# Performance work log

Measured on AMD Instinct MI355X. Metric: run time of the kernel, lower is better.

## Reference

```python
import jax, jax.numpy as jnp
import numpy as np

N_NODES = 100000
N_EDGES = 1600000
F_NODE = 32
F_EDGE = 32
HID = 64
N_TGT = 32


def setup_inputs() -> dict:
    key = jax.random.key(0)
    ks = jax.random.split(key, 12)
    x = jax.random.normal(ks[0], (N_NODES, F_NODE), dtype=jnp.float32)
    edge_index = jax.random.randint(ks[1], (2, N_EDGES), 0, N_NODES, dtype=jnp.int64)
    edge_attr = jax.random.normal(ks[2], (N_EDGES, F_EDGE), dtype=jnp.float32)
    u = jax.random.normal(ks[3], (1, 8), dtype=jnp.float32)
    batch = jnp.zeros((N_NODES,), dtype=jnp.int64)
    s1 = 1.0 / np.sqrt(F_NODE + F_EDGE)
    s2 = 1.0 / np.sqrt(HID)
    s3 = 1.0 / np.sqrt(HID + F_NODE)
    W1a = jax.random.uniform(ks[4], (F_NODE + F_EDGE, HID), jnp.float32, -s1, s1)
    b1a = jax.random.uniform(ks[5], (HID,), jnp.float32, -s1, s1)
    W1b = jax.random.uniform(ks[6], (HID, HID), jnp.float32, -s2, s2)
    b1b = jax.random.uniform(ks[7], (HID,), jnp.float32, -s2, s2)
    W2a = jax.random.uniform(ks[8], (HID + F_NODE, HID), jnp.float32, -s3, s3)
    b2a = jax.random.uniform(ks[9], (HID,), jnp.float32, -s3, s3)
    W2b = jax.random.uniform(ks[10], (HID, N_TGT), jnp.float32, -s2, s2)
    b2b = jax.random.uniform(ks[11], (N_TGT,), jnp.float32, -s2, s2)
    return {"x": x, "edge_index": edge_index, "edge_attr": edge_attr, "u": u,
            "batch": batch, "W1a": W1a, "b1a": b1a, "W1b": W1b, "b1b": b1b,
            "W2a": W2a, "b2a": b2a, "W2b": W2b, "b2b": b2b}


def reference(x, edge_index, edge_attr, u, batch,
              W1a, b1a, W1b, b1b, W2a, b2a, W2b, b2b):
    row, col = edge_index[0], edge_index[1]
    n = x.shape[0]
    # gather source node features and concat with edge features -> edge MLP
    m = jnp.concatenate([x[col], edge_attr], axis=1)           # [E, F_NODE+F_EDGE]
    m = jax.nn.relu(m @ W1a + b1a) @ W1b + b1b                  # [E, HID]
    # scatter-mean back to destination nodes (row)
    summed = jax.ops.segment_sum(m, row, num_segments=n)        # [N, HID]
    counts = jax.ops.segment_sum(jnp.ones((m.shape[0],), m.dtype), row, num_segments=n)
    agg = summed / jnp.maximum(counts, 1.0)[:, None]
    h = jnp.concatenate([x, agg], axis=1)                       # [N, HID+F_NODE]
    out = jax.nn.relu(h @ W2a + b2a) @ W2b + b2b                # [N, N_TGT]
    return out
```

## Files before the change

kernel.cpp:

```cpp
#include <hip/hip_runtime.h>

#define NN 100000
#define NE 1600000
#define NB ((NN + 255) / 256)
#define TPW 8

typedef unsigned int uint32;
typedef float f32x4 __attribute__((ext_vector_type(4)));
typedef short bf16x8 __attribute__((ext_vector_type(8)));

__device__ __forceinline__ float bflo(uint32 u) { return __uint_as_float(u << 16); }
__device__ __forceinline__ float bfhi(uint32 u) { return __uint_as_float(u & 0xffff0000u); }
__device__ __forceinline__ uint32 bfbits(float v) { return (__float_as_uint(v) + 0x8000u) >> 16; }
__device__ __forceinline__ uint32 pack2(float a, float b) { return bfbits(a) | (bfbits(b) << 16); }

__device__ __forceinline__ int sigma_ch(int c) {
    return (((c >> 2) & 3) << 4) + (((c >> 4) & 3) << 2) + (c & 3);
}

__global__ __launch_bounds__(256) void k_hist_rank(const int* __restrict__ ei, int* __restrict__ deg,
                                                   int* __restrict__ pos, int E) {
    int e = blockIdx.x * 256 + threadIdx.x;
    if (e < E) pos[e] = atomicAdd(&deg[ei[e]], 1);
}

__global__ __launch_bounds__(256) void k_hist(const int* __restrict__ ei, int* __restrict__ deg, int E) {
    int e = blockIdx.x * 256 + threadIdx.x;
    if (e < E) atomicAdd(&deg[ei[e]], 1);
}

__global__ __launch_bounds__(256) void k_scan1(const int* __restrict__ deg, int* __restrict__ offs,
                                               int* __restrict__ bsums, int n) {
    __shared__ int s[256];
    int tid = threadIdx.x;
    int i = blockIdx.x * 256 + tid;
    int v = (i < n) ? deg[i] : 0;
    int acc = v;
    s[tid] = acc;
    __syncthreads();
    #pragma unroll
    for (int off = 1; off < 256; off <<= 1) {
        int t = (tid >= off) ? s[tid - off] : 0;
        __syncthreads();
        acc += t;
        s[tid] = acc;
        __syncthreads();
    }
    if (i < n) offs[i] = acc - v;
    if (tid == 255) bsums[blockIdx.x] = acc;
}

__global__ __launch_bounds__(512) void k_scan2(int* __restrict__ bsums, int nb) {
    __shared__ int s[512];
    int tid = threadIdx.x;
    int v = (tid < nb) ? bsums[tid] : 0;
    int acc = v;
    s[tid] = acc;
    __syncthreads();
    #pragma unroll
    for (int off = 1; off < 512; off <<= 1) {
        int t = (tid >= off) ? s[tid - off] : 0;
        __syncthreads();
        acc += t;
        s[tid] = acc;
        __syncthreads();
    }
    bsums[tid] = acc - v;
}

__global__ __launch_bounds__(256) void k_pos(const int* __restrict__ ei, const int* __restrict__ offs,
                                             const int* __restrict__ bsums, int* __restrict__ pos, int E) {
    int e = blockIdx.x * 256 + threadIdx.x;
    if (e >= E) return;
    int r = ei[e];
    pos[e] += offs[r] + bsums[r >> 8];
}

__global__ __launch_bounds__(256) void k_prep2(const float* __restrict__ W1b, const float* __restrict__ b1b,
                                               const float* __restrict__ W2a, const float* __restrict__ W1a,
                                               const float* __restrict__ x,
                                               float* __restrict__ Wc, float* __restrict__ bc,
                                               uint4* __restrict__ wpack, uint32* __restrict__ xbw,
                                               int perm) {
    int idx = blockIdx.x * 256 + threadIdx.x;
    if (idx < 4096) {
        int r = idx >> 6, c = idx & 63;
        float a = 0.f;
        for (int k = 0; k < 64; ++k) a += W1b[r * 64 + k] * W2a[(32 + k) * 64 + c];
        int rs = perm ? sigma_ch(r) : r;
        Wc[rs * 64 + c] = a;
        if (idx < 64) {
            float bacc = 0.f;
            for (int k = 0; k < 64; ++k) bacc += b1b[k] * W2a[(32 + k) * 64 + idx];
            bc[idx] = bacc;
        }
        if (idx < 512) {
            int table = idx >> 8;
            int cc = (idx >> 6) & 3;
            int lane = idx & 63;
            int qq = lane >> 4, en = lane & 15;
            int ch = cc * 16 + en;
            uint32 w[4];
            #pragma unroll
            for (int j = 0; j < 4; ++j) {
                int row0 = (table ? 0 : 32) + qq * 8 + j * 2;
                w[j] = pack2(W1a[row0 * 64 + ch], W1a[(row0 + 1) * 64 + ch]);
            }
            wpack[idx] = make_uint4(w[0], w[1], w[2], w[3]);
        }
    }
    int xi = idx - 4096;
    if (xi >= 0 && xi < NN * 16) {
        float2 v = *(const float2*)(x + (size_t)2 * xi);
        xbw[xi] = pack2(v.x, v.y);
    }
}

__global__ __launch_bounds__(256) void k_edge_mfma(
    const int* __restrict__ ei, const float* __restrict__ ea, const uint32* __restrict__ xbw,
    const uint4* __restrict__ wpack, const float* __restrict__ b1a,
    const int* __restrict__ pos, uint32* __restrict__ g)
{
    int lane = threadIdx.x & 63;
    int wave = threadIdx.x >> 6;
    int en = lane & 15;
    int qq = lane >> 4;

    union U { uint4 u; bf16x8 v; };
    U wB[4], wA[4];
    #pragma unroll
    for (int cc = 0; cc < 4; ++cc) {
        wB[cc].u = wpack[cc * 64 + lane];
        wA[cc].u = wpack[256 + cc * 64 + lane];
    }
    f32x4 binit[4];
    #pragma unroll
    for (int cc = 0; cc < 4; ++cc) {
        float4 b = *(const float4*)(b1a + cc * 16 + qq * 4);
        binit[cc] = (f32x4){b.x, b.y, b.z, b.w};
    }

    int base = blockIdx.x * (64 * TPW) + wave * (16 * TPW);

    int e0 = base + en;
    int p0 = pos[e0];
    int c0 = ei[NE + e0];
    float4 f0a = *(const float4*)(ea + (size_t)e0 * 32 + qq * 8);
    float4 f0b = *(const float4*)(ea + (size_t)e0 * 32 + qq * 8 + 4);

    int e1 = base + 16 + en;
    int p1 = pos[e1];
    int c1 = ei[NE + e1];
    float4 f1a = *(const float4*)(ea + (size_t)e1 * 32 + qq * 8);
    float4 f1b = *(const float4*)(ea + (size_t)e1 * 32 + qq * 8 + 4);

    uint4 xv0 = *(const uint4*)(xbw + (size_t)c0 * 16 + qq * 4);

    #pragma unroll 1
    for (int t = 0; t < TPW; ++t) {
        int e2 = base + (t + 2) * 16 + en;
        if (e2 > NE - 1) e2 = NE - 1;
        int p2 = pos[e2];
        int c2 = ei[NE + e2];
        float4 f2a = *(const float4*)(ea + (size_t)e2 * 32 + qq * 8);
        float4 f2b = *(const float4*)(ea + (size_t)e2 * 32 + qq * 8 + 4);
        uint4 xv1 = *(const uint4*)(xbw + (size_t)c1 * 16 + qq * 4);

        U bea, bx;
        bea.u.x = pack2(f0a.x, f0a.y);
        bea.u.y = pack2(f0a.z, f0a.w);
        bea.u.z = pack2(f0b.x, f0b.y);
        bea.u.w = pack2(f0b.z, f0b.w);
        bx.u = xv0;

        f32x4 acc[4];
        #pragma unroll
        for (int cc = 0; cc < 4; ++cc) acc[cc] = binit[cc];
        #pragma unroll
        for (int cc = 0; cc < 4; ++cc)
            acc[cc] = __builtin_amdgcn_mfma_f32_16x16x32_bf16(wB[cc].v, bea.v, acc[cc], 0, 0, 0);
        #pragma unroll
        for (int cc = 0; cc < 4; ++cc)
            acc[cc] = __builtin_amdgcn_mfma_f32_16x16x32_bf16(wA[cc].v, bx.v, acc[cc], 0, 0, 0);

        uint4 o0, o1;
        o0.x = pack2(fmaxf(acc[0][0], 0.f), fmaxf(acc[0][1], 0.f));
        o0.y = pack2(fmaxf(acc[0][2], 0.f), fmaxf(acc[0][3], 0.f));
        o0.z = pack2(fmaxf(acc[1][0], 0.f), fmaxf(acc[1][1], 0.f));
        o0.w = pack2(fmaxf(acc[1][2], 0.f), fmaxf(acc[1][3], 0.f));
        o1.x = pack2(fmaxf(acc[2][0], 0.f), fmaxf(acc[2][1], 0.f));
        o1.y = pack2(fmaxf(acc[2][2], 0.f), fmaxf(acc[2][3], 0.f));
        o1.z = pack2(fmaxf(acc[3][0], 0.f), fmaxf(acc[3][1], 0.f));
        o1.w = pack2(fmaxf(acc[3][2], 0.f), fmaxf(acc[3][3], 0.f));
        uint4* gp = (uint4*)(g + (size_t)p0 * 32 + qq * 8);
        gp[0] = o0;
        gp[1] = o1;

        p0 = p1; f0a = f1a; f0b = f1b; xv0 = xv1;
        p1 = p2; c1 = c2; f1a = f2a; f1b = f2b;
    }
}

__global__ __launch_bounds__(256) void k_seg_c(
    const int* __restrict__ deg, const int* __restrict__ offs, const int* __restrict__ bsums,
    const uint32* __restrict__ g, float* __restrict__ Sacc)
{
    int node = blockIdx.x * 4 + (threadIdx.x >> 6);
    if (node >= NN) return;
    int lane = threadIdx.x & 63;
    int quarter = lane >> 4;
    int wi = lane & 15;
    int d = deg[node];
    size_t start = (size_t)(offs[node] + bsums[node >> 8]);

    float4 S = {0.f, 0.f, 0.f, 0.f};
    int r = quarter;
    for (; r + 4 < d; r += 8) {
        uint2 u1 = *(const uint2*)(g + (start + r) * 32 + wi * 2);
        uint2 u2 = *(const uint2*)(g + (start + r + 4) * 32 + wi * 2);
        S.x += bflo(u1.x) + bflo(u2.x);
        S.y += bfhi(u1.x) + bfhi(u2.x);
        S.z += bflo(u1.y) + bflo(u2.y);
        S.w += bfhi(u1.y) + bfhi(u2.y);
    }
    if (r < d) {
        uint2 u = *(const uint2*)(g + (start + r) * 32 + wi * 2);
        S.x += bflo(u.x); S.y += bfhi(u.x); S.z += bflo(u.y); S.w += bfhi(u.y);
    }
    S.x += __shfl_xor(S.x, 16); S.y += __shfl_xor(S.y, 16);
    S.z += __shfl_xor(S.z, 16); S.w += __shfl_xor(S.w, 16);
    S.x += __shfl_xor(S.x, 32); S.y += __shfl_xor(S.y, 32);
    S.z += __shfl_xor(S.z, 32); S.w += __shfl_xor(S.w, 32);
    if (quarter == 0)
        *(float4*)(Sacc + (size_t)node * 64 + wi * 4) = make_float4(S.x, S.y, S.z, S.w);
}

__global__ __launch_bounds__(256) void k_edge_atom(
    const float* __restrict__ x, const int* __restrict__ ei, const float* __restrict__ ea,
    const float* __restrict__ W1a, const float* __restrict__ b1a,
    float* __restrict__ Sacc, int E)
{
    __shared__ float sWB[32 * 64];
    __shared__ float sWA[32 * 64];
    __shared__ float sb[64];
    for (int t = threadIdx.x; t < 32 * 64; t += 256) {
        sWB[t] = W1a[32 * 64 + t];
        sWA[t] = W1a[t];
    }
    if (threadIdx.x < 64) sb[threadIdx.x] = b1a[threadIdx.x];
    __syncthreads();
    int e = blockIdx.x * 256 + threadIdx.x;
    if (e >= E) return;
    int row = ei[e];
    int col = ei[NE + e];
    float h[64];
    #pragma unroll
    for (int j = 0; j < 64; ++j) h[j] = sb[j];
    const float4* xrow = (const float4*)(x + (size_t)col * 32);
    #pragma unroll
    for (int k4 = 0; k4 < 8; ++k4) {
        float4 v = xrow[k4];
        float vv[4] = {v.x, v.y, v.z, v.w};
        #pragma unroll
        for (int c = 0; c < 4; ++c) {
            float val = vv[c];
            const float4* wr = (const float4*)&sWA[(k4 * 4 + c) * 64];
            #pragma unroll
            for (int j4 = 0; j4 < 16; ++j4) {
                float4 w = wr[j4];
                h[j4 * 4 + 0] += val * w.x; h[j4 * 4 + 1] += val * w.y;
                h[j4 * 4 + 2] += val * w.z; h[j4 * 4 + 3] += val * w.w;
            }
        }
    }
    const float4* earow = (const float4*)(ea + (size_t)e * 32);
    #pragma unroll
    for (int k4 = 0; k4 < 8; ++k4) {
        float4 v = earow[k4];
        float vv[4] = {v.x, v.y, v.z, v.w};
        #pragma unroll
        for (int c = 0; c < 4; ++c) {
            float val = vv[c];
            const float4* wr = (const float4*)&sWB[(k4 * 4 + c) * 64];
            #pragma unroll
            for (int j4 = 0; j4 < 16; ++j4) {
                float4 w = wr[j4];
                h[j4 * 4 + 0] += val * w.x; h[j4 * 4 + 1] += val * w.y;
                h[j4 * 4 + 2] += val * w.z; h[j4 * 4 + 3] += val * w.w;
            }
        }
    }
    float* srow = Sacc + (size_t)row * 64;
    #pragma unroll
    for (int j = 0; j < 64; ++j) atomicAdd(&srow[j], fmaxf(h[j], 0.f));
}

__global__ __launch_bounds__(256) void k_node(
    const float* __restrict__ x, const float* __restrict__ Sacc, const int* __restrict__ deg,
    const float* __restrict__ Wc, const float* __restrict__ bc,
    const float* __restrict__ W2a, const float* __restrict__ b2a,
    const float* __restrict__ W2b, const float* __restrict__ b2b,
    float* __restrict__ out, int N)
{
    __shared__ float sWc[64 * 64];
    __shared__ float sW2ax[32 * 64];
    __shared__ float sW2b[64 * 32];
    __shared__ float sbc2[64];
    __shared__ float sb2[64];
    __shared__ float sb2b_[32];
    for (int t = threadIdx.x; t < 64 * 64; t += 256) sWc[t] = Wc[t];
    for (int t = threadIdx.x; t < 32 * 64; t += 256) sW2ax[t] = W2a[t];
    for (int t = threadIdx.x; t < 64 * 32; t += 256) sW2b[t] = W2b[t];
    if (threadIdx.x < 64) {
        sbc2[threadIdx.x] = bc[threadIdx.x] + b2a[threadIdx.x];
        sb2[threadIdx.x] = b2a[threadIdx.x];
    }
    if (threadIdx.x < 32) sb2b_[threadIdx.x] = b2b[threadIdx.x];
    __syncthreads();

    int i = blockIdx.x * 256 + threadIdx.x;
    if (i >= N) return;
    int d = deg[i];
    float inv = (d > 0) ? 1.f / (float)d : 0.f;

    float h2[64];
    #pragma unroll
    for (int j = 0; j < 64; ++j) h2[j] = (d > 0) ? sbc2[j] : sb2[j];

    const float4* sp = (const float4*)(Sacc + (size_t)i * 64);
    #pragma unroll 2
    for (int k4 = 0; k4 < 16; ++k4) {
        float4 v = sp[k4];
        float vv[4] = {v.x * inv, v.y * inv, v.z * inv, v.w * inv};
        #pragma unroll
        for (int c = 0; c < 4; ++c) {
            float val = vv[c];
            const float4* wr = (const float4*)&sWc[(k4 * 4 + c) * 64];
            #pragma unroll
            for (int j4 = 0; j4 < 16; ++j4) {
                float4 w = wr[j4];
                h2[j4 * 4 + 0] += val * w.x; h2[j4 * 4 + 1] += val * w.y;
                h2[j4 * 4 + 2] += val * w.z; h2[j4 * 4 + 3] += val * w.w;
            }
        }
    }
    const float4* xrow = (const float4*)(x + (size_t)i * 32);
    #pragma unroll 2
    for (int k4 = 0; k4 < 8; ++k4) {
        float4 v = xrow[k4];
        float vv[4] = {v.x, v.y, v.z, v.w};
        #pragma unroll
        for (int c = 0; c < 4; ++c) {
            float val = vv[c];
            const float4* wr = (const float4*)&sW2ax[(k4 * 4 + c) * 64];
            #pragma unroll
            for (int j4 = 0; j4 < 16; ++j4) {
                float4 w = wr[j4];
                h2[j4 * 4 + 0] += val * w.x; h2[j4 * 4 + 1] += val * w.y;
                h2[j4 * 4 + 2] += val * w.z; h2[j4 * 4 + 3] += val * w.w;
            }
        }
    }
    #pragma unroll
    for (int j = 0; j < 64; ++j) h2[j] = fmaxf(h2[j], 0.f);

    float o[32];
    #pragma unroll
    for (int j = 0; j < 32; ++j) o[j] = sb2b_[j];
    #pragma unroll
    for (int k = 0; k < 64; ++k) {
        float val = h2[k];
        const float4* wr = (const float4*)&sW2b[k * 32];
        #pragma unroll
        for (int j4 = 0; j4 < 8; ++j4) {
            float4 w = wr[j4];
            o[j4 * 4 + 0] += val * w.x; o[j4 * 4 + 1] += val * w.y;
            o[j4 * 4 + 2] += val * w.z; o[j4 * 4 + 3] += val * w.w;
        }
    }
    float4* orow = (float4*)(out + (size_t)i * 32);
    #pragma unroll
    for (int q = 0; q < 8; ++q)
        orow[q] = make_float4(o[q * 4], o[q * 4 + 1], o[q * 4 + 2], o[q * 4 + 3]);
}

extern "C" void kernel_launch(void* const* d_in, const int* in_sizes, int n_in,
                              void* d_out, int out_size, void* d_ws, size_t ws_size,
                              hipStream_t stream) {
    const float* x   = (const float*)d_in[0];
    const int*   ei  = (const int*)d_in[1];
    const float* ea  = (const float*)d_in[2];
    const float* W1a = (const float*)d_in[5];
    const float* b1a = (const float*)d_in[6];
    const float* W1b = (const float*)d_in[7];
    const float* b1b = (const float*)d_in[8];
    const float* W2a = (const float*)d_in[9];
    const float* b2a = (const float*)d_in[10];
    const float* W2b = (const float*)d_in[11];
    const float* b2b = (const float*)d_in[12];
    float* out = (float*)d_out;

    char* p = (char*)d_ws;
    int* deg        = (int*)p;        p += (size_t)NN * 4;
    int* offs       = (int*)p;        p += (size_t)NN * 4;
    int* bsums      = (int*)p;        p += 2048;
    float* Wc       = (float*)p;      p += 4096 * 4;
    float* bc       = (float*)p;      p += 64 * 4;
    uint4* wpack    = (uint4*)p;      p += 512 * 16;
    int* pos        = (int*)p;        p += (size_t)NE * 4;
    uint32* xbw     = (uint32*)p;     p += (size_t)NN * 16 * 4;
    float* Sacc     = (float*)p;      p += (size_t)NN * 64 * 4;
    size_t off_g    = (size_t)(p - (char*)d_ws);
    uint32* g       = (uint32*)p;
    size_t need     = off_g + (size_t)NE * 128;

    dim3 blk(256);
    int prep_grid = (4096 + NN * 16 + 255) / 256;

    if (ws_size >= need) {
        hipMemsetAsync(deg, 0, (size_t)NN * 4, stream);
        hipLaunchKernelGGL(k_hist_rank, dim3((NE + 255) / 256), blk, 0, stream, ei, deg, pos, NE);
        hipLaunchKernelGGL(k_scan1, dim3(NB), blk, 0, stream, deg, offs, bsums, NN);
        hipLaunchKernelGGL(k_scan2, dim3(1), dim3(512), 0, stream, bsums, NB);
        hipLaunchKernelGGL(k_pos, dim3((NE + 255) / 256), blk, 0, stream, ei, offs, bsums, pos, NE);
        hipLaunchKernelGGL(k_prep2, dim3(prep_grid), blk, 0, stream,
                           W1b, b1b, W2a, W1a, x, Wc, bc, wpack, xbw, 1);
        hipLaunchKernelGGL(k_edge_mfma, dim3(NE / (64 * TPW)), blk, 0, stream,
                           ei, ea, xbw, wpack, b1a, pos, g);
        hipLaunchKernelGGL(k_seg_c, dim3((NN + 3) / 4), blk, 0, stream, deg, offs, bsums, g, Sacc);
        hipLaunchKernelGGL(k_node, dim3(NB), blk, 0, stream,
                           x, Sacc, deg, Wc, bc, W2a, b2a, W2b, b2b, out, NN);
    } else {
        hipMemsetAsync(deg, 0, (size_t)NN * 4, stream);
        hipMemsetAsync(Sacc, 0, (size_t)NN * 64 * 4, stream);
        hipLaunchKernelGGL(k_hist, dim3((NE + 255) / 256), blk, 0, stream, ei, deg, NE);
        hipLaunchKernelGGL(k_prep2, dim3(prep_grid), blk, 0, stream,
                           W1b, b1b, W2a, W1a, x, Wc, bc, wpack, xbw, 0);
        hipLaunchKernelGGL(k_edge_atom, dim3((NE + 255) / 256), blk, 0, stream,
                           x, ei, ea, W1a, b1a, Sacc, NE);
        hipLaunchKernelGGL(k_node, dim3(NB), blk, 0, stream,
                           x, Sacc, deg, Wc, bc, W2a, b2a, W2b, b2b, out, NN);
    }
}
```

Measured before the change: 306.1 us.

## Fuse histogram with prep, fold position fixup into edge kernel, fuse segment-reduce with node MLP

Merges the rank histogram and weight/x packing into one launch, drops the separate k_pos pass by computing each edge's sorted position inside the edge MFMA kernel from rank, offs and bsums, and fuses the segment-mean reduction with the node MLP in a persistent kernel. This removes several launches and the Sacc round-trip through global memory. The cost is extra indirect loads in the edge kernel, and a fused node kernel that does its scalar FMA MLP per wave using weights held in LDS. In the fallback path the rank array is now written even though it is unused.

```diff
diff --git a/kernel.cpp b/kernel.cpp
--- a/kernel.cpp
+++ b/kernel.cpp
@@ -4,6 +4,8 @@
 #define NE 1600000
 #define NB ((NN + 255) / 256)
 #define TPW 8
+#define HB ((NE + 255) / 256)
+#define PB ((4096 + NN * 16 + 255) / 256)
 
 typedef unsigned int uint32;
 typedef float f32x4 __attribute__((ext_vector_type(4)));
@@ -18,71 +20,20 @@
     return (((c >> 2) & 3) << 4) + (((c >> 4) & 3) << 2) + (c & 3);
 }
 
-__global__ __launch_bounds__(256) void k_hist_rank(const int* __restrict__ ei, int* __restrict__ deg,
-                                                   int* __restrict__ pos, int E) {
-    int e = blockIdx.x * 256 + threadIdx.x;
-    if (e < E) pos[e] = atomicAdd(&deg[ei[e]], 1);
-}
-
-__global__ __launch_bounds__(256) void k_hist(const int* __restrict__ ei, int* __restrict__ deg, int E) {
-    int e = blockIdx.x * 256 + threadIdx.x;
-    if (e < E) atomicAdd(&deg[ei[e]], 1);
-}
-
-__global__ __launch_bounds__(256) void k_scan1(const int* __restrict__ deg, int* __restrict__ offs,
-                                               int* __restrict__ bsums, int n) {
-    __shared__ int s[256];
-    int tid = threadIdx.x;
-    int i = blockIdx.x * 256 + tid;
-    int v = (i < n) ? deg[i] : 0;
-    int acc = v;
-    s[tid] = acc;
-    __syncthreads();
-    #pragma unroll
-    for (int off = 1; off < 256; off <<= 1) {
-        int t = (tid >= off) ? s[tid - off] : 0;
-        __syncthreads();
-        acc += t;
-        s[tid] = acc;
-        __syncthreads();
-    }
-    if (i < n) offs[i] = acc - v;
-    if (tid == 255) bsums[blockIdx.x] = acc;
-}
-
-__global__ __launch_bounds__(512) void k_scan2(int* __restrict__ bsums, int nb) {
-    __shared__ int s[512];
-    int tid = threadIdx.x;
-    int v = (tid < nb) ? bsums[tid] : 0;
-    int acc = v;
-    s[tid] = acc;
-    __syncthreads();
-    #pragma unroll
-    for (int off = 1; off < 512; off <<= 1) {
-        int t = (tid >= off) ? s[tid - off] : 0;
-        __syncthreads();
-        acc += t;
-        s[tid] = acc;
-        __syncthreads();
-    }
-    bsums[tid] = acc - v;
-}
-
-__global__ __launch_bounds__(256) void k_pos(const int* __restrict__ ei, const int* __restrict__ offs,
-                                             const int* __restrict__ bsums, int* __restrict__ pos, int E) {
-    int e = blockIdx.x * 256 + threadIdx.x;
-    if (e >= E) return;
-    int r = ei[e];
-    pos[e] += offs[r] + bsums[r >> 8];
-}
-
-__global__ __launch_bounds__(256) void k_prep2(const float* __restrict__ W1b, const float* __restrict__ b1b,
-                                               const float* __restrict__ W2a, const float* __restrict__ W1a,
-                                               const float* __restrict__ x,
-                                               float* __restrict__ Wc, float* __restrict__ bc,
-                                               uint4* __restrict__ wpack, uint32* __restrict__ xbw,
-                                               int perm) {
-    int idx = blockIdx.x * 256 + threadIdx.x;
+__global__ __launch_bounds__(256) void k_hist_prep(
+    const int* __restrict__ ei, int* __restrict__ deg, int* __restrict__ rank,
+    const float* __restrict__ W1b, const float* __restrict__ b1b,
+    const float* __restrict__ W2a, const float* __restrict__ W1a, const float* __restrict__ x,
+    float* __restrict__ Wc, float* __restrict__ bc,
+    uint4* __restrict__ wpack, uint32* __restrict__ xbw, int perm)
+{
+    int b = blockIdx.x;
+    if (b < HB) {
+        int e = b * 256 + threadIdx.x;
+        if (e < NE) rank[e] = atomicAdd(&deg[ei[e]], 1);
+        return;
+    }
+    int idx = (b - HB) * 256 + threadIdx.x;
     if (idx < 4096) {
         int r = idx >> 6, c = idx & 63;
         float a = 0.f;
@@ -116,10 +67,50 @@
     }
 }
 
+__global__ __launch_bounds__(256) void k_scan1(const int* __restrict__ deg, int* __restrict__ offs,
+                                               int* __restrict__ bsums, int n) {
+    __shared__ int s[256];
+    int tid = threadIdx.x;
+    int i = blockIdx.x * 256 + tid;
+    int v = (i < n) ? deg[i] : 0;
+    int acc = v;
+    s[tid] = acc;
+    __syncthreads();
+    #pragma unroll
+    for (int off = 1; off < 256; off <<= 1) {
+        int t = (tid >= off) ? s[tid - off] : 0;
+        __syncthreads();
+        acc += t;
+        s[tid] = acc;
+        __syncthreads();
+    }
+    if (i < n) offs[i] = acc - v;
+    if (tid == 255) bsums[blockIdx.x] = acc;
+}
+
+__global__ __launch_bounds__(512) void k_scan2(int* __restrict__ bsums, int nb) {
+    __shared__ int s[512];
+    int tid = threadIdx.x;
+    int v = (tid < nb) ? bsums[tid] : 0;
+    int acc = v;
+    s[tid] = acc;
+    __syncthreads();
+    #pragma unroll
+    for (int off = 1; off < 512; off <<= 1) {
+        int t = (tid >= off) ? s[tid - off] : 0;
+        __syncthreads();
+        acc += t;
+        s[tid] = acc;
+        __syncthreads();
+    }
+    bsums[tid] = acc - v;
+}
+
 __global__ __launch_bounds__(256) void k_edge_mfma(
     const int* __restrict__ ei, const float* __restrict__ ea, const uint32* __restrict__ xbw,
     const uint4* __restrict__ wpack, const float* __restrict__ b1a,
-    const int* __restrict__ pos, uint32* __restrict__ g)
+    const int* __restrict__ rank, const int* __restrict__ offs, const int* __restrict__ bsums,
+    uint32* __restrict__ g)
 {
     int lane = threadIdx.x & 63;
     int wave = threadIdx.x >> 6;
@@ -143,14 +134,17 @@
     int base = blockIdx.x * (64 * TPW) + wave * (16 * TPW);
 
     int e0 = base + en;
-    int p0 = pos[e0];
+    int r0 = ei[e0];
     int c0 = ei[NE + e0];
+    int k0 = rank[e0];
     float4 f0a = *(const float4*)(ea + (size_t)e0 * 32 + qq * 8);
     float4 f0b = *(const float4*)(ea + (size_t)e0 * 32 + qq * 8 + 4);
+    int p0 = k0 + offs[r0] + bsums[r0 >> 8];
 
     int e1 = base + 16 + en;
-    int p1 = pos[e1];
+    int r1 = ei[e1];
     int c1 = ei[NE + e1];
+    int k1 = rank[e1];
     float4 f1a = *(const float4*)(ea + (size_t)e1 * 32 + qq * 8);
     float4 f1b = *(const float4*)(ea + (size_t)e1 * 32 + qq * 8 + 4);
 
@@ -160,10 +154,12 @@
     for (int t = 0; t < TPW; ++t) {
         int e2 = base + (t + 2) * 16 + en;
         if (e2 > NE - 1) e2 = NE - 1;
-        int p2 = pos[e2];
+        int r2 = ei[e2];
         int c2 = ei[NE + e2];
+        int k2 = rank[e2];
         float4 f2a = *(const float4*)(ea + (size_t)e2 * 32 + qq * 8);
         float4 f2b = *(const float4*)(ea + (size_t)e2 * 32 + qq * 8 + 4);
+        int p1 = k1 + offs[r1] + bsums[r1 >> 8];
         uint4 xv1 = *(const uint4*)(xbw + (size_t)c1 * 16 + qq * 4);
 
         U bea, bx;
@@ -197,42 +193,94 @@
         gp[1] = o1;
 
         p0 = p1; f0a = f1a; f0b = f1b; xv0 = xv1;
-        p1 = p2; c1 = c2; f1a = f2a; f1b = f2b;
-    }
-}
-
-__global__ __launch_bounds__(256) void k_seg_c(
+        r1 = r2; c1 = c2; k1 = k2; f1a = f2a; f1b = f2b;
+    }
+}
+
+#define SN_BLOCKS 2048
+__global__ __launch_bounds__(256) void k_segnode(
     const int* __restrict__ deg, const int* __restrict__ offs, const int* __restrict__ bsums,
-    const uint32* __restrict__ g, float* __restrict__ Sacc)
+    const uint32* __restrict__ g, const float* __restrict__ x,
+    const float* __restrict__ Wc, const float* __restrict__ bc,
+    const float* __restrict__ W2a, const float* __restrict__ b2a,
+    const float* __restrict__ W2b, const float* __restrict__ b2b,
+    float* __restrict__ out)
 {
-    int node = blockIdx.x * 4 + (threadIdx.x >> 6);
-    if (node >= NN) return;
+    __shared__ float sWc[64 * 64];
+    __shared__ float sW2ax[32 * 64];
+    __shared__ float sW2b[64 * 32];
+    __shared__ float sbc2[64];
+    __shared__ float sb2[64];
+    __shared__ float sb2b_[32];
+    for (int t = threadIdx.x; t < 64 * 64; t += 256) sWc[t] = Wc[t];
+    for (int t = threadIdx.x; t < 32 * 64; t += 256) sW2ax[t] = W2a[t];
+    for (int t = threadIdx.x; t < 64 * 32; t += 256) sW2b[t] = W2b[t];
+    if (threadIdx.x < 64) {
+        sbc2[threadIdx.x] = bc[threadIdx.x] + b2a[threadIdx.x];
+        sb2[threadIdx.x] = b2a[threadIdx.x];
+    }
+    if (threadIdx.x < 32) sb2b_[threadIdx.x] = b2b[threadIdx.x];
+    __syncthreads();
+
     int lane = threadIdx.x & 63;
+    int wave = threadIdx.x >> 6;
     int quarter = lane >> 4;
     int wi = lane & 15;
-    int d = deg[node];
-    size_t start = (size_t)(offs[node] + bsums[node >> 8]);
-
-    float4 S = {0.f, 0.f, 0.f, 0.f};
-    int r = quarter;
-    for (; r + 4 < d; r += 8) {
-        uint2 u1 = *(const uint2*)(g + (start + r) * 32 + wi * 2);
-        uint2 u2 = *(const uint2*)(g + (start + r + 4) * 32 + wi * 2);
-        S.x += bflo(u1.x) + bflo(u2.x);
-        S.y += bfhi(u1.x) + bfhi(u2.x);
-        S.z += bflo(u1.y) + bflo(u2.y);
-        S.w += bfhi(u1.y) + bfhi(u2.y);
-    }
-    if (r < d) {
-        uint2 u = *(const uint2*)(g + (start + r) * 32 + wi * 2);
-        S.x += bflo(u.x); S.y += bfhi(u.x); S.z += bflo(u.y); S.w += bfhi(u.y);
-    }
-    S.x += __shfl_xor(S.x, 16); S.y += __shfl_xor(S.y, 16);
-    S.z += __shfl_xor(S.z, 16); S.w += __shfl_xor(S.w, 16);
-    S.x += __shfl_xor(S.x, 32); S.y += __shfl_xor(S.y, 32);
-    S.z += __shfl_xor(S.z, 32); S.w += __shfl_xor(S.w, 32);
-    if (quarter == 0)
-        *(float4*)(Sacc + (size_t)node * 64 + wi * 4) = make_float4(S.x, S.y, S.z, S.w);
+
+    for (int node = blockIdx.x * 4 + wave; node < NN; node += SN_BLOCKS * 4) {
+        int d = deg[node];
+        size_t start = (size_t)(offs[node] + bsums[node >> 8]);
+
+        float4 S = {0.f, 0.f, 0.f, 0.f};
+        int r = quarter;
+        for (; r + 4 < d; r += 8) {
+            uint2 u1 = *(const uint2*)(g + (start + r) * 32 + wi * 2);
+            uint2 u2 = *(const uint2*)(g + (start + r + 4) * 32 + wi * 2);
+            S.x += bflo(u1.x) + bflo(u2.x);
+            S.y += bfhi(u1.x) + bfhi(u2.x);
+            S.z += bflo(u1.y) + bflo(u2.y);
+            S.w += bfhi(u1.y) + bfhi(u2.y);
+        }
+        if (r < d) {
+            uint2 u = *(const uint2*)(g + (start + r) * 32 + wi * 2);
+            S.x += bflo(u.x); S.y += bfhi(u.x); S.z += bflo(u.y); S.w += bfhi(u.y);
+        }
+        S.x += __shfl_xor(S.x, 16); S.y += __shfl_xor(S.y, 16);
+        S.z += __shfl_xor(S.z, 16); S.w += __shfl_xor(S.w, 16);
+        S.x += __shfl_xor(S.x, 32); S.y += __shfl_xor(S.y, 32);
+        S.z += __shfl_xor(S.z, 32); S.w += __shfl_xor(S.w, 32);
+        float inv = (d > 0) ? 1.f / (float)d : 0.f;
+        S.x *= inv; S.y *= inv; S.z *= inv; S.w *= inv;
+
+        int j = lane;
+        float h = (d > 0) ? sbc2[j] : sb2[j];
+        #pragma unroll
+        for (int k = 0; k < 64; k += 4) {
+            float s0 = __shfl(S.x, k >> 2);
+            float s1 = __shfl(S.y, k >> 2);
+            float s2 = __shfl(S.z, k >> 2);
+            float s3 = __shfl(S.w, k >> 2);
+            h += s0 * sWc[(k + 0) * 64 + j];
+            h += s1 * sWc[(k + 1) * 64 + j];
+            h += s2 * sWc[(k + 2) * 64 + j];
+            h += s3 * sWc[(k + 3) * 64 + j];
+        }
+        const float* xrow = x + (size_t)node * 32;
+        #pragma unroll
+        for (int k = 0; k < 32; ++k) h += xrow[k] * sW2ax[k * 64 + j];
+        h = fmaxf(h, 0.f);
+
+        int jo = lane & 31;
+        int half = lane >> 5;
+        float o = 0.f;
+        #pragma unroll
+        for (int kk = 0; kk < 32; ++kk) {
+            float hk = __shfl(h, half * 32 + kk);
+            o += hk * sW2b[(half * 32 + kk) * 32 + jo];
+        }
+        o += __shfl_xor(o, 32);
+        if (lane < 32) out[(size_t)node * 32 + jo] = o + sb2b_[jo];
+    }
 }
 
 __global__ __launch_bounds__(256) void k_edge_atom(
@@ -407,7 +455,7 @@
     float* Wc       = (float*)p;      p += 4096 * 4;
     float* bc       = (float*)p;      p += 64 * 4;
     uint4* wpack    = (uint4*)p;      p += 512 * 16;
-    int* pos        = (int*)p;        p += (size_t)NE * 4;
+    int* rank       = (int*)p;        p += (size_t)NE * 4;
     uint32* xbw     = (uint32*)p;     p += (size_t)NN * 16 * 4;
     float* Sacc     = (float*)p;      p += (size_t)NN * 64 * 4;
     size_t off_g    = (size_t)(p - (char*)d_ws);
@@ -415,27 +463,22 @@
     size_t need     = off_g + (size_t)NE * 128;
 
     dim3 blk(256);
-    int prep_grid = (4096 + NN * 16 + 255) / 256;
 
     if (ws_size >= need) {
         hipMemsetAsync(deg, 0, (size_t)NN * 4, stream);
-        hipLaunchKernelGGL(k_hist_rank, dim3((NE + 255) / 256), blk, 0, stream, ei, deg, pos, NE);
+        hipLaunchKernelGGL(k_hist_prep, dim3(HB + PB), blk, 0, stream,
+                           ei, deg, rank, W1b, b1b, W2a, W1a, x, Wc, bc, wpack, xbw, 1);
         hipLaunchKernelGGL(k_scan1, dim3(NB), blk, 0, stream, deg, offs, bsums, NN);
         hipLaunchKernelGGL(k_scan2, dim3(1), dim3(512), 0, stream, bsums, NB);
-        hipLaunchKernelGGL(k_pos, dim3((NE + 255) / 256), blk, 0, stream, ei, offs, bsums, pos, NE);
-        hipLaunchKernelGGL(k_prep2, dim3(prep_grid), blk, 0, stream,
-                           W1b, b1b, W2a, W1a, x, Wc, bc, wpack, xbw, 1);
         hipLaunchKernelGGL(k_edge_mfma, dim3(NE / (64 * TPW)), blk, 0, stream,
-                           ei, ea, xbw, wpack, b1a, pos, g);
-        hipLaunchKernelGGL(k_seg_c, dim3((NN + 3) / 4), blk, 0, stream, deg, offs, bsums, g, Sacc);
-        hipLaunchKernelGGL(k_node, dim3(NB), blk, 0, stream,
-                           x, Sacc, deg, Wc, bc, W2a, b2a, W2b, b2b, out, NN);
+                           ei, ea, xbw, wpack, b1a, rank, offs, bsums, g);
+        hipLaunchKernelGGL(k_segnode, dim3(SN_BLOCKS), blk, 0, stream,
+                           deg, offs, bsums, g, x, Wc, bc, W2a, b2a, W2b, b2b, out);
     } else {
         hipMemsetAsync(deg, 0, (size_t)NN * 4, stream);
         hipMemsetAsync(Sacc, 0, (size_t)NN * 64 * 4, stream);
-        hipLaunchKernelGGL(k_hist, dim3((NE + 255) / 256), blk, 0, stream, ei, deg, NE);
-        hipLaunchKernelGGL(k_prep2, dim3(prep_grid), blk, 0, stream,
-                           W1b, b1b, W2a, W1a, x, Wc, bc, wpack, xbw, 0);
+        hipLaunchKernelGGL(k_hist_prep, dim3(HB + PB), blk, 0, stream,
+                           ei, deg, rank, W1b, b1b, W2a, W1a, x, Wc, bc, wpack, xbw, 0);
         hipLaunchKernelGGL(k_edge_atom, dim3((NE + 255) / 256), blk, 0, stream,
                            x, ei, ea, W1a, b1a, Sacc, NE);
         hipLaunchKernelGGL(k_node, dim3(NB), blk, 0, stream,
```

New measurement: 409.4 us. 1.34x slower.
